# Kernel tuning notes

Measured on AMD Instinct MI355X. Metric: run time of the kernel, lower is better.

## Reference

```python
import jax, jax.numpy as jnp
import numpy as np

DIM = 2048
N_HEADS = 32
N_KV_HEADS = 8
HEAD_DIM = DIM // N_HEADS
N_REP = N_HEADS // N_KV_HEADS
BSZ, SEQ = 2, 2048


def setup_inputs() -> dict:
    key = jax.random.key(0)
    ks = jax.random.split(key, 6)
    hidden_states = jax.random.normal(ks[0], (BSZ, SEQ, DIM), jnp.float32)
    # additive causal mask [1,1,S,S]
    causal = jnp.tril(jnp.ones((SEQ, SEQ), jnp.bool_))
    attention_mask = jnp.where(causal, 0.0, -1e9).astype(jnp.float32)[None, None]
    # RoPE tables [S, head_dim]
    inv_freq = 1.0 / (10000.0 ** (np.arange(0, HEAD_DIM, 2, dtype=np.float32) / HEAD_DIM))
    t = np.arange(SEQ, dtype=np.float32)
    freqs = np.outer(t, inv_freq)  # [S, head_dim/2]
    emb = np.concatenate([freqs, freqs], axis=-1)  # [S, head_dim]
    position_cos = jnp.asarray(np.cos(emb), jnp.float32)
    position_sin = jnp.asarray(np.sin(emb), jnp.float32)
    s = 0.02
    Wq = jax.random.normal(ks[1], (DIM, DIM), jnp.float32) * s
    Wk = jax.random.normal(ks[2], (N_KV_HEADS * HEAD_DIM, DIM), jnp.float32) * s
    Wv = jax.random.normal(ks[3], (N_KV_HEADS * HEAD_DIM, DIM), jnp.float32) * s
    Wo = jax.random.normal(ks[4], (DIM, DIM), jnp.float32) * s
    return {"hidden_states": hidden_states, "attention_mask": attention_mask,
            "position_cos": position_cos, "position_sin": position_sin,
            "Wq": Wq, "Wk": Wk, "Wv": Wv, "Wo": Wo}


def _rotate_half(x):
    x1, x2 = jnp.split(x, 2, axis=-1)
    return jnp.concatenate([-x2, x1], axis=-1)


def _apply_rope(x, cos, sin):
    # x: [b, h, s, d]; cos/sin: [s, d] broadcast over (b, h)
    return x * cos + _rotate_half(x) * sin


def reference(hidden_states, attention_mask, position_cos, position_sin, Wq, Wk, Wv, Wo):
    b, s, _ = hidden_states.shape
    q = jnp.einsum('bsd,ed->bse', hidden_states, Wq).reshape(b, s, N_HEADS, HEAD_DIM).transpose(0, 2, 1, 3)
    k = jnp.einsum('bsd,ed->bse', hidden_states, Wk).reshape(b, s, N_KV_HEADS, HEAD_DIM).transpose(0, 2, 1, 3)
    v = jnp.einsum('bsd,ed->bse', hidden_states, Wv).reshape(b, s, N_KV_HEADS, HEAD_DIM).transpose(0, 2, 1, 3)
    q = _apply_rope(q, position_cos, position_sin)
    k = _apply_rope(k, position_cos, position_sin)
    # GQA: group query heads over kv heads instead of physically repeating k/v
    qg = q.reshape(b, N_KV_HEADS, N_REP, s, HEAD_DIM)
    scores = jnp.einsum('bgrqd,bgkd->bgrqk', qg, k) * (1.0 / jnp.sqrt(jnp.float32(HEAD_DIM)))
    scores = scores + attention_mask[:, :, None, :s, :s]
    weights = jax.nn.softmax(scores.astype(jnp.float32), axis=-1).astype(q.dtype)
    attn = jnp.einsum('bgrqk,bgkd->bgrqd', weights, v)
    attn = attn.reshape(b, N_HEADS, s, HEAD_DIM).transpose(0, 2, 1, 3).reshape(b, s, DIM)
    out = jnp.einsum('bsd,ed->bse', attn, Wo)
    return out
```

## Files before the change

kernel.cpp:

```cpp
#include <hip/hip_runtime.h>
#include <math.h>

#define BSZ 2
#define SEQ 2048
#define DIM 2048
#define NH 32
#define NKV 8
#define HD 64
#define KVDIM 512

typedef short short8 __attribute__((ext_vector_type(8)));
typedef short short4v __attribute__((ext_vector_type(4)));
typedef float f32x4 __attribute__((ext_vector_type(4)));
typedef int i32x4 __attribute__((ext_vector_type(4)));

__device__ __forceinline__ short fbf(float x) {
    unsigned u = __float_as_uint(x);
    u = (u + 0x7fffu + ((u >> 16) & 1u)) >> 16;
    return (short)u;
}

#define AS1(p) ((const __attribute__((address_space(1))) void*)(p))
#define AS3(p) ((__attribute__((address_space(3))) void*)(p))

#if defined(__has_builtin)
#if __has_builtin(__builtin_amdgcn_permlane16_swap) && __has_builtin(__builtin_amdgcn_permlane32_swap)
#define HAVE_PERMLANE 1
#endif
#endif

__device__ __forceinline__ float redmax4(float x) {
#ifdef HAVE_PERMLANE
    {
        auto p = __builtin_amdgcn_permlane16_swap(__float_as_uint(x), __float_as_uint(x), false, false);
        x = fmaxf(__uint_as_float(p[0]), __uint_as_float(p[1]));
    }
    {
        auto p = __builtin_amdgcn_permlane32_swap(__float_as_uint(x), __float_as_uint(x), false, false);
        x = fmaxf(__uint_as_float(p[0]), __uint_as_float(p[1]));
    }
#else
    x = fmaxf(x, __shfl_xor(x, 16));
    x = fmaxf(x, __shfl_xor(x, 32));
#endif
    return x;
}
__device__ __forceinline__ float redsum4(float x) {
#ifdef HAVE_PERMLANE
    {
        auto p = __builtin_amdgcn_permlane16_swap(__float_as_uint(x), __float_as_uint(x), false, false);
        x = __uint_as_float(p[0]) + __uint_as_float(p[1]);
    }
    {
        auto p = __builtin_amdgcn_permlane32_swap(__float_as_uint(x), __float_as_uint(x), false, false);
        x = __uint_as_float(p[0]) + __uint_as_float(p[1]);
    }
#else
    x += __shfl_xor(x, 16);
    x += __shfl_xor(x, 32);
#endif
    return x;
}

__global__ __launch_bounds__(256) void prep(const float* __restrict__ X,
                                            const float* __restrict__ Wq,
                                            const float* __restrict__ Wk,
                                            const float* __restrict__ Wv,
                                            const float* __restrict__ Wo,
                                            short* __restrict__ Xb,
                                            short* __restrict__ Wqkv,
                                            short* __restrict__ Wob) {
    int i = blockIdx.x * 256 + threadIdx.x;
    const float* src; short* dst; int j;
    if (i < 2097152)      { src = X;  dst = Xb;             j = i; }
    else if (i < 3145728) { src = Wq; dst = Wqkv;           j = i - 2097152; }
    else if (i < 3407872) { src = Wk; dst = Wqkv + 4194304; j = i - 3145728; }
    else if (i < 3670016) { src = Wv; dst = Wqkv + 5242880; j = i - 3407872; }
    else                  { src = Wo; dst = Wob;            j = i - 3670016; }
    float4 f = ((const float4*)src)[j];
    short4v s = { fbf(f.x), fbf(f.y), fbf(f.z), fbf(f.w) };
    ((short4v*)dst)[j] = s;
}

__global__ __launch_bounds__(256) void gemm_qkv(const short* __restrict__ A,
                                                const short* __restrict__ W,
                                                const float* __restrict__ cosT,
                                                const float* __restrict__ sinT,
                                                short* __restrict__ Qo,
                                                short* __restrict__ Ko,
                                                short* __restrict__ Vo) {
    __shared__ short SM[2 * 128 * 64];
    short* As = SM;
    short* Bs = SM + 128 * 64;
    const int K = 2048;
    const int tid = threadIdx.x;
    const int lane = tid & 63, wave = tid >> 6;
    const int l15 = lane & 15, quad = lane >> 4;
    const int m0 = blockIdx.y * 128, n0 = blockIdx.x * 128;
    const int wm = (wave >> 1) * 64, wn = (wave & 1) * 64;
    f32x4 acc[4][4] = {};
    int srow[4], gcol[4];
#pragma unroll
    for (int v = 0; v < 4; ++v) {
        int s = v * 256 + tid;
        srow[v] = s >> 3;
        gcol[v] = ((s & 7) ^ (srow[v] & 7)) * 8;
    }
    for (int kb = 0; kb < K; kb += 64) {
        __syncthreads();
#pragma unroll
        for (int v = 0; v < 4; ++v) {
            int s = v * 256 + tid;
            __builtin_amdgcn_global_load_lds(AS1(A + (size_t)(m0 + srow[v]) * K + kb + gcol[v]),
                                             AS3(&As[s * 8]), 16, 0, 0);
            __builtin_amdgcn_global_load_lds(AS1(W + (size_t)(n0 + srow[v]) * K + kb + gcol[v]),
                                             AS3(&Bs[s * 8]), 16, 0, 0);
        }
        __syncthreads();
#pragma unroll
        for (int kh = 0; kh < 2; ++kh) {
            const int cs = ((kh * 4 + quad) ^ (l15 & 7)) * 8;
            short8 af[4], bf8[4];
#pragma unroll
            for (int i = 0; i < 4; ++i)
                af[i] = *(const short8*)&As[(wm + i * 16 + l15) * 64 + cs];
#pragma unroll
            for (int j = 0; j < 4; ++j)
                bf8[j] = *(const short8*)&Bs[(wn + j * 16 + l15) * 64 + cs];
#pragma unroll
            for (int i = 0; i < 4; ++i)
#pragma unroll
                for (int j = 0; j < 4; ++j)
                    acc[i][j] = __builtin_amdgcn_mfma_f32_16x16x32_bf16(af[i], bf8[j], acc[i][j], 0, 0, 0);
        }
    }
    __syncthreads();
    const int n0r = n0 + wn;
    if (n0r < 2560) {
        short* dst; int heads, hh; float scale;
        if (n0r < 2048) { dst = Qo; heads = NH;  hh = n0r >> 6;          scale = 0.125f * 1.44269504088896f; }
        else            { dst = Ko; heads = NKV; hh = (n0r - 2048) >> 6; scale = 1.0f; }
        short* EB = SM + wave * 4096;
#pragma unroll
        for (int i = 0; i < 4; ++i)
#pragma unroll
            for (int r = 0; r < 4; ++r) {
                int rr = i * 16 + quad * 4 + r;
                int s = (m0 + wm + rr) & (SEQ - 1);
                int msk = ((rr >> 1) & 7) * 8;
#pragma unroll
                for (int jp = 0; jp < 2; ++jp) {
                    int d1 = jp * 16 + l15;
                    float c1 = cosT[s * HD + d1], s1v = sinT[s * HD + d1];
                    float x1 = acc[i][jp][r], x2 = acc[i][jp + 2][r];
                    EB[rr * 64 + (d1 ^ msk)]        = fbf((x1 * c1 - x2 * s1v) * scale);
                    EB[rr * 64 + ((d1 + 32) ^ msk)] = fbf((x2 * c1 + x1 * s1v) * scale);
                }
            }
#pragma unroll
        for (int t = 0; t < 8; ++t) {
            int rr = (lane >> 3) + t * 8;
            int c = lane & 7;
            short8 v8 = *(const short8*)&EB[rr * 64 + c * 8];
            int dchunk = c ^ ((rr >> 1) & 7);
            int mrow = m0 + wm + rr;
            int s = mrow & (SEQ - 1), bb = mrow >> 11;
            *(short8*)&dst[((size_t)(bb * SEQ + s) * heads + hh) * HD + dchunk * 8] = v8;
        }
    } else {
        const int hh = (n0r - 2560) >> 6;
#pragma unroll
        for (int i = 0; i < 4; ++i) {
            int mrow4 = m0 + wm + i * 16 + quad * 4;
            int s_abs = mrow4 & (SEQ - 1);
            int bb = mrow4 >> 11;
            int blk = s_abs >> 6, kk = s_abs & 63;
            int ob = ((kk >> 5) << 3) | (((kk >> 2) & 3) << 1) | ((kk >> 4) & 1);
#pragma unroll
            for (int j = 0; j < 4; ++j) {
                int d = j * 16 + l15;
                short4v pk = { fbf(acc[i][j][0]), fbf(acc[i][j][1]),
                               fbf(acc[i][j][2]), fbf(acc[i][j][3]) };
                *(short4v*)&Vo[(((size_t)(bb * NKV + hh) * HD + d) * SEQ) + blk * 64 + ob * 4] = pk;
            }
        }
    }
}

__global__ __launch_bounds__(256) void gemm_bf16(const short* __restrict__ A,
                                                 const short* __restrict__ W,
                                                 float* __restrict__ C,
                                                 int M, int N, int K) {
    __shared__ short As[128 * 64];
    __shared__ short Bs[128 * 64];
    const int tid = threadIdx.x;
    const int lane = tid & 63, wave = tid >> 6;
    const int l15 = lane & 15, quad = lane >> 4;
    const int m0 = blockIdx.y * 128, n0 = blockIdx.x * 128;
    const int wm = (wave >> 1) * 64, wn = (wave & 1) * 64;
    f32x4 acc[4][4] = {};
    int srow[4], gcol[4];
#pragma unroll
    for (int v = 0; v < 4; ++v) {
        int s = v * 256 + tid;
        srow[v] = s >> 3;
        gcol[v] = ((s & 7) ^ (srow[v] & 7)) * 8;
    }
    for (int kb = 0; kb < K; kb += 64) {
        __syncthreads();
#pragma unroll
        for (int v = 0; v < 4; ++v) {
            int s = v * 256 + tid;
            __builtin_amdgcn_global_load_lds(AS1(A + (size_t)(m0 + srow[v]) * K + kb + gcol[v]),
                                             AS3(&As[s * 8]), 16, 0, 0);
            __builtin_amdgcn_global_load_lds(AS1(W + (size_t)(n0 + srow[v]) * K + kb + gcol[v]),
                                             AS3(&Bs[s * 8]), 16, 0, 0);
        }
        __syncthreads();
#pragma unroll
        for (int kh = 0; kh < 2; ++kh) {
            const int cs = ((kh * 4 + quad) ^ (l15 & 7)) * 8;
            short8 af[4], bf8[4];
#pragma unroll
            for (int i = 0; i < 4; ++i)
                af[i] = *(const short8*)&As[(wm + i * 16 + l15) * 64 + cs];
#pragma unroll
            for (int j = 0; j < 4; ++j)
                bf8[j] = *(const short8*)&Bs[(wn + j * 16 + l15) * 64 + cs];
#pragma unroll
            for (int i = 0; i < 4; ++i)
#pragma unroll
                for (int j = 0; j < 4; ++j)
                    acc[i][j] = __builtin_amdgcn_mfma_f32_16x16x32_bf16(af[i], bf8[j], acc[i][j], 0, 0, 0);
        }
    }
#pragma unroll
    for (int i = 0; i < 4; ++i)
#pragma unroll
        for (int j = 0; j < 4; ++j)
#pragma unroll
            for (int r = 0; r < 4; ++r)
                C[(size_t)(m0 + wm + i * 16 + quad * 4 + r) * N + n0 + wn + j * 16 + l15] = acc[i][j][r];
}

__global__ __launch_bounds__(512, 4) void flash4(const short* __restrict__ Qb,
                                                 const short* __restrict__ Kb,
                                                 const short* __restrict__ VT,
                                                 short* __restrict__ O) {
    __shared__ short Ks[2][128 * 64];
    __shared__ short Vs[2][64 * 128];
    const int d = blockIdx.x + blockIdx.y * 64;
    const int bh = (d & 255) >> 2;
    const int qt = (d < 256) ? 7 - (d & 3) : (d & 3);
    const int b = bh >> 5, h = bh & 31, kvh = h >> 2;
    const int tid = threadIdx.x;
    const int wave = tid >> 6, lane = tid & 63;
    const int l15 = lane & 15, quad = lane >> 4;

    short8 qf[2][2];
#pragma unroll
    for (int g = 0; g < 2; ++g) {
        const short* qp = Qb + ((size_t)b * SEQ + qt * 256 + g * 128 + wave * 16 + l15) * DIM + h * HD + quad * 8;
        qf[g][0] = *(const short8*)qp;
        qf[g][1] = *(const short8*)(qp + 32);
    }
    f32x4 o[2][4] = {};
    float m[2] = {-1e30f, -1e30f}, l[2] = {0.f, 0.f};

    const short* Kbase = Kb + (size_t)b * SEQ * KVDIM + kvh * HD;
    const short* Vbase = VT + (size_t)(b * NKV + kvh) * HD * SEQ;

    int krow[2], kcol[2], vrow[2], vcol[2];
#pragma unroll
    for (int v = 0; v < 2; ++v) {
        int s = v * 512 + tid;
        krow[v] = s >> 3;
        kcol[v] = ((s & 7) ^ (krow[v] & 7)) * 8;
        vrow[v] = s >> 4;
        vcol[v] = ((s & 15) ^ (vrow[v] & 7)) * 8;
    }
    auto issue = [&](int kt, int bi) {
#pragma unroll
        for (int v = 0; v < 2; ++v) {
            int s = v * 512 + tid;
            __builtin_amdgcn_global_load_lds(AS1(Kbase + (size_t)(kt * 128 + krow[v]) * KVDIM + kcol[v]),
                                             AS3(&Ks[bi][s * 8]), 16, 0, 0);
            __builtin_amdgcn_global_load_lds(AS1(Vbase + (size_t)vrow[v] * SEQ + kt * 128 + vcol[v]),
                                             AS3(&Vs[bi][s * 8]), 16, 0, 0);
        }
    };
    issue(0, 0);
    const int nkt = 2 * qt + 2;
    for (int kt = 0; kt < nkt; ++kt) {
        const int bi = kt & 1;
        __syncthreads();
        if (kt + 1 < nkt) issue(kt + 1, bi ^ 1);

#pragma unroll
        for (int g = 0; g < 2; ++g) {
            const int qmin = qt * 256 + g * 128 + wave * 16;
            if (kt * 128 > qmin + 15) continue;
            f32x4 st[8] = {};
#pragma unroll
            for (int kh = 0; kh < 2; ++kh) {
                const int cs = ((kh * 4 + quad) ^ (l15 & 7)) * 8;
#pragma unroll
                for (int nt = 0; nt < 8; ++nt) {
                    short8 ka = *(const short8*)&Ks[bi][(nt * 16 + l15) * 64 + cs];
                    st[nt] = __builtin_amdgcn_mfma_f32_16x16x32_bf16(ka, qf[g][kh], st[nt], 0, 0, 0);
                }
            }
            if (kt * 128 + 127 > qmin) {
                const int q = qmin + l15;
#pragma unroll
                for (int nt = 0; nt < 8; ++nt)
                    if (kt * 128 + nt * 16 + 15 > qmin) {
#pragma unroll
                        for (int r = 0; r < 4; ++r)
                            if (kt * 128 + nt * 16 + quad * 4 + r > q) st[nt][r] = -1e30f;
                    }
            }
            float mnt[8];
#pragma unroll
            for (int nt = 0; nt < 8; ++nt)
                mnt[nt] = fmaxf(fmaxf(fmaxf(st[nt][0], st[nt][1]), st[nt][2]), st[nt][3]);
            float ma = fmaxf(fmaxf(mnt[0], mnt[1]), mnt[2]);
            float mb = fmaxf(fmaxf(mnt[3], mnt[4]), mnt[5]);
            float mc = fmaxf(fmaxf(mnt[6], mnt[7]), ma);
            float mx = redmax4(fmaxf(mb, mc));

            const bool noskip = !__all(mx <= m[g]);
            float mn = m[g];
            float al = 1.0f;
            float alr[4];
            if (noskip) {
                mn = fmaxf(m[g], mx);
                al = __builtin_amdgcn_exp2f(m[g] - mn);
                m[g] = mn;
#pragma unroll
                for (int r = 0; r < 4; ++r) alr[r] = __shfl(al, quad * 4 + r);
            }
            i32x4 aw[4];
            f32x4 rs4 = {};
#pragma unroll
            for (int nt = 0; nt < 8; ++nt) {
                f32x4 pv;
#pragma unroll
                for (int r = 0; r < 4; ++r) pv[r] = __builtin_amdgcn_exp2f(st[nt][r] - mn);
                rs4 += pv;
                unsigned u0 = __float_as_uint(pv[0]) + 0x8000u;
                unsigned u1 = __float_as_uint(pv[1]) + 0x8000u;
                unsigned u2 = __float_as_uint(pv[2]) + 0x8000u;
                unsigned u3 = __float_as_uint(pv[3]) + 0x8000u;
                aw[nt >> 1][(nt & 1) * 2 + 0] = (int)__builtin_amdgcn_perm(u1, u0, 0x07060302u);
                aw[nt >> 1][(nt & 1) * 2 + 1] = (int)__builtin_amdgcn_perm(u3, u2, 0x07060302u);
            }
            float rs = redsum4((rs4[0] + rs4[1]) + (rs4[2] + rs4[3]));
            l[g] = l[g] * al + rs;
            if (noskip) {
#pragma unroll
                for (int dt = 0; dt < 4; ++dt) {
                    o[g][dt][0] *= alr[0]; o[g][dt][1] *= alr[1];
                    o[g][dt][2] *= alr[2]; o[g][dt][3] *= alr[3];
                }
            }
#pragma unroll
            for (int dt = 0; dt < 4; ++dt) {
                f32x4 t = o[g][dt];
#pragma unroll
                for (int kh = 0; kh < 4; ++kh) {
                    const int slot = (kh * 4 + quad) ^ (l15 & 7);
                    short8 vf = *(const short8*)&Vs[bi][(dt * 16 + l15) * 128 + slot * 8];
                    t = __builtin_amdgcn_mfma_f32_16x16x32_bf16(__builtin_bit_cast(short8, aw[kh]), vf, t, 0, 0, 0);
                }
                o[g][dt] = t;
            }
        }
    }
#pragma unroll
    for (int g = 0; g < 2; ++g) {
        float li = 1.0f / l[g];
        float lr[4];
#pragma unroll
        for (int r = 0; r < 4; ++r) lr[r] = __shfl(li, quad * 4 + r);
        short* Oo = O + ((size_t)b * SEQ + qt * 256 + g * 128 + wave * 16 + quad * 4) * DIM + h * HD + l15;
#pragma unroll
        for (int r = 0; r < 4; ++r)
#pragma unroll
            for (int dt = 0; dt < 4; ++dt)
                Oo[(size_t)r * DIM + dt * 16] = fbf(o[g][dt][r] * lr[r]);
    }
}

extern "C" void kernel_launch(void* const* d_in, const int* in_sizes, int n_in,
                              void* d_out, int out_size, void* d_ws, size_t ws_size,
                              hipStream_t stream) {
    const float* X    = (const float*)d_in[0];
    const float* cosT = (const float*)d_in[2];
    const float* sinT = (const float*)d_in[3];
    const float* Wq   = (const float*)d_in[4];
    const float* Wk   = (const float*)d_in[5];
    const float* Wv   = (const float*)d_in[6];
    const float* Wo   = (const float*)d_in[7];

    char* ws = (char*)d_ws;
    short* Xb    = (short*)(ws);
    short* ATTb  = Xb;
    short* WQKVb = (short*)(ws + 16777216);
    short* Wob   = (short*)(ws + 29360128);
    short* Qbb   = (short*)(ws + 37748736);
    short* Kbb   = (short*)(ws + 54525952);
    short* VTb   = (short*)(ws + 58720256);

    const int M = BSZ * SEQ;
    dim3 blk(256);

    prep<<<dim3(18432), blk, 0, stream>>>(X, Wq, Wk, Wv, Wo, Xb, WQKVb, Wob);
    gemm_qkv<<<dim3(24, M / 128), blk, 0, stream>>>(Xb, WQKVb, cosT, sinT, Qbb, Kbb, VTb);
    flash4<<<dim3(64, 8), dim3(512), 0, stream>>>(Qbb, Kbb, VTb, ATTb);
    gemm_bf16<<<dim3(DIM / 128, M / 128), blk, 0, stream>>>(ATTb, Wob, (float*)d_out, M, DIM, DIM);
}
```

Before: 320.8 us.

## Rewrite QKV GEMM with 256x256 tiles and 4-stage async LDS pipeline

The fused QKV projection GEMM now uses 512-thread blocks computing 256x256 tiles, with each wave owning a 128x64 sub-tile. Global-to-LDS loads run through a 4-deep ring of 32-wide K slices, controlled by explicit vmcnt waits and one barrier per step, replacing the previous two-barrier synchronous loop. The grid is flattened to 192 blocks with an XCD-aware remap of block ids, and s_setprio is raised around the MFMA burst. The aim is to hide load latency and raise operand reuse. In exchange it uses 128KB of LDS and more accumulator registers per thread, and 192 blocks may leave some CUs idle.

```diff
diff --git a/kernel.cpp b/kernel.cpp
--- a/kernel.cpp
+++ b/kernel.cpp
@@ -82,67 +82,96 @@
     ((short4v*)dst)[j] = s;
 }
 
-__global__ __launch_bounds__(256) void gemm_qkv(const short* __restrict__ A,
-                                                const short* __restrict__ W,
-                                                const float* __restrict__ cosT,
-                                                const float* __restrict__ sinT,
-                                                short* __restrict__ Qo,
-                                                short* __restrict__ Ko,
-                                                short* __restrict__ Vo) {
-    __shared__ short SM[2 * 128 * 64];
-    short* As = SM;
-    short* Bs = SM + 128 * 64;
+__global__ __launch_bounds__(512, 2) void gemm_qkv(const short* __restrict__ A,
+                                                   const short* __restrict__ W,
+                                                   const float* __restrict__ cosT,
+                                                   const float* __restrict__ sinT,
+                                                   short* __restrict__ Qo,
+                                                   short* __restrict__ Ko,
+                                                   short* __restrict__ Vo) {
+    __shared__ short SM[65536];
     const int K = 2048;
+    const int NT = 64;
     const int tid = threadIdx.x;
     const int lane = tid & 63, wave = tid >> 6;
     const int l15 = lane & 15, quad = lane >> 4;
-    const int m0 = blockIdx.y * 128, n0 = blockIdx.x * 128;
-    const int wm = (wave >> 1) * 64, wn = (wave & 1) * 64;
-    f32x4 acc[4][4] = {};
-    int srow[4], gcol[4];
-#pragma unroll
-    for (int v = 0; v < 4; ++v) {
-        int s = v * 256 + tid;
-        srow[v] = s >> 3;
-        gcol[v] = ((s & 7) ^ (srow[v] & 7)) * 8;
-    }
-    for (int kb = 0; kb < K; kb += 64) {
-        __syncthreads();
-#pragma unroll
-        for (int v = 0; v < 4; ++v) {
-            int s = v * 256 + tid;
-            __builtin_amdgcn_global_load_lds(AS1(A + (size_t)(m0 + srow[v]) * K + kb + gcol[v]),
-                                             AS3(&As[s * 8]), 16, 0, 0);
-            __builtin_amdgcn_global_load_lds(AS1(W + (size_t)(n0 + srow[v]) * K + kb + gcol[v]),
-                                             AS3(&Bs[s * 8]), 16, 0, 0);
-        }
-        __syncthreads();
-#pragma unroll
-        for (int kh = 0; kh < 2; ++kh) {
-            const int cs = ((kh * 4 + quad) ^ (l15 & 7)) * 8;
-            short8 af[4], bf8[4];
-#pragma unroll
-            for (int i = 0; i < 4; ++i)
-                af[i] = *(const short8*)&As[(wm + i * 16 + l15) * 64 + cs];
+    const int wm = (wave >> 2) * 128;
+    const int wn = (wave & 3) * 64;
+    const int orig = blockIdx.x;
+    const int wgid = (orig & 7) * 24 + (orig >> 3);
+    const int by = wgid / 12, bx = wgid - by * 12;
+    const int m0 = by * 256, n0 = bx * 256;
+
+    size_t aoff[2], boff[2]; int lslot[2];
+#pragma unroll
+    for (int v = 0; v < 2; ++v) {
+        int s = v * 512 + tid;
+        int pr = s >> 3, w = s & 7;
+        int row = (pr << 1) | (w & 1);
+        int c = (w >> 1) ^ (pr & 3);
+        aoff[v] = (size_t)(m0 + row) * K + c * 8;
+        boff[v] = (size_t)(n0 + row) * K + c * 8;
+        lslot[v] = s * 8;
+    }
+    const int r0a = wm + l15;
+    const int pa = r0a >> 1;
+    const int slotA0 = pa * 8 + (((quad ^ (pa & 3)) << 1) | (r0a & 1));
+    const int r0b = wn + l15;
+    const int pb = r0b >> 1;
+    const int slotB0 = pb * 8 + (((quad ^ (pb & 3)) << 1) | (r0b & 1));
+
+    f32x4 acc[8][4] = {};
+
+    auto issue = [&](int t) {
+        const int kb = t * 32;
+        short* Ad = SM + (t & 3) * 8192;
+        short* Bd = SM + 32768 + (t & 3) * 8192;
+#pragma unroll
+        for (int v = 0; v < 2; ++v) {
+            __builtin_amdgcn_global_load_lds(AS1(A + aoff[v] + kb), AS3(Ad + lslot[v]), 16, 0, 0);
+            __builtin_amdgcn_global_load_lds(AS1(W + boff[v] + kb), AS3(Bd + lslot[v]), 16, 0, 0);
+        }
+    };
+    issue(0); issue(1); issue(2);
+    asm volatile("s_waitcnt vmcnt(8)" ::: "memory");
+    __builtin_amdgcn_s_barrier();
+    asm volatile("" ::: "memory");
+    __builtin_amdgcn_sched_barrier(0);
+
+    for (int t = 0; t < NT; ++t) {
+        if (t < NT - 3) issue(t + 3);
+        const short* Ab = SM + (t & 3) * 8192;
+        const short* Bb = SM + 32768 + (t & 3) * 8192;
+        short8 af[8], bf8[4];
+#pragma unroll
+        for (int j = 0; j < 4; ++j)
+            bf8[j] = *(const short8*)&Bb[(slotB0 + j * 64) * 8];
+#pragma unroll
+        for (int i = 0; i < 8; ++i)
+            af[i] = *(const short8*)&Ab[(slotA0 + i * 64) * 8];
+        __builtin_amdgcn_s_setprio(1);
+#pragma unroll
+        for (int i = 0; i < 8; ++i)
 #pragma unroll
             for (int j = 0; j < 4; ++j)
-                bf8[j] = *(const short8*)&Bs[(wn + j * 16 + l15) * 64 + cs];
-#pragma unroll
-            for (int i = 0; i < 4; ++i)
-#pragma unroll
-                for (int j = 0; j < 4; ++j)
-                    acc[i][j] = __builtin_amdgcn_mfma_f32_16x16x32_bf16(af[i], bf8[j], acc[i][j], 0, 0, 0);
-        }
-    }
-    __syncthreads();
+                acc[i][j] = __builtin_amdgcn_mfma_f32_16x16x32_bf16(af[i], bf8[j], acc[i][j], 0, 0, 0);
+        __builtin_amdgcn_s_setprio(0);
+        if (t < NT - 3)       asm volatile("s_waitcnt vmcnt(8)" ::: "memory");
+        else if (t == NT - 3) asm volatile("s_waitcnt vmcnt(4)" ::: "memory");
+        else if (t == NT - 2) asm volatile("s_waitcnt vmcnt(0)" ::: "memory");
+        __builtin_amdgcn_s_barrier();
+        asm volatile("" ::: "memory");
+        __builtin_amdgcn_sched_barrier(0);
+    }
+
     const int n0r = n0 + wn;
     if (n0r < 2560) {
         short* dst; int heads, hh; float scale;
         if (n0r < 2048) { dst = Qo; heads = NH;  hh = n0r >> 6;          scale = 0.125f * 1.44269504088896f; }
         else            { dst = Ko; heads = NKV; hh = (n0r - 2048) >> 6; scale = 1.0f; }
-        short* EB = SM + wave * 4096;
-#pragma unroll
-        for (int i = 0; i < 4; ++i)
+        short* EB = SM + wave * 8192;
+#pragma unroll
+        for (int i = 0; i < 8; ++i)
 #pragma unroll
             for (int r = 0; r < 4; ++r) {
                 int rr = i * 16 + quad * 4 + r;
@@ -158,7 +187,7 @@
                 }
             }
 #pragma unroll
-        for (int t = 0; t < 8; ++t) {
+        for (int t = 0; t < 16; ++t) {
             int rr = (lane >> 3) + t * 8;
             int c = lane & 7;
             short8 v8 = *(const short8*)&EB[rr * 64 + c * 8];
@@ -170,7 +199,7 @@
     } else {
         const int hh = (n0r - 2560) >> 6;
 #pragma unroll
-        for (int i = 0; i < 4; ++i) {
+        for (int i = 0; i < 8; ++i) {
             int mrow4 = m0 + wm + i * 16 + quad * 4;
             int s_abs = mrow4 & (SEQ - 1);
             int bb = mrow4 >> 11;
@@ -416,7 +445,7 @@
     dim3 blk(256);
 
     prep<<<dim3(18432), blk, 0, stream>>>(X, Wq, Wk, Wv, Wo, Xb, WQKVb, Wob);
-    gemm_qkv<<<dim3(24, M / 128), blk, 0, stream>>>(Xb, WQKVb, cosT, sinT, Qbb, Kbb, VTb);
+    gemm_qkv<<<dim3(192), dim3(512), 0, stream>>>(Xb, WQKVb, cosT, sinT, Qbb, Kbb, VTb);
     flash4<<<dim3(64, 8), dim3(512), 0, stream>>>(Qbb, Kbb, VTb, ATTb);
     gemm_bf16<<<dim3(DIM / 128, M / 128), blk, 0, stream>>>(ATTb, Wob, (float*)d_out, M, DIM, DIM);
 }
```

Result: faster. 307.5 us (-4.2%).
